# Kernel optimization log

Measured on AMD Instinct MI355X. Metric: run time of the kernel, lower is better.

Reference implementation:

```python
import jax, jax.numpy as jnp
import numpy as np

HIDDEN = 1024
HEADS = 16
HEAD_DIM = HIDDEN // HEADS
NEG_INF = -1.0e9


def setup_inputs() -> dict:
    key = jax.random.key(0)
    ks = jax.random.split(key, 9)
    B, S = 4, 2048
    scale = 1.0 / np.sqrt(HIDDEN)
    inp = {
        'query': jax.random.normal(ks[0], (B, S, HIDDEN), dtype=jnp.float32),
        'masks': jnp.ones((B, S), dtype=jnp.float32),
        'Wq': jax.random.normal(ks[1], (HIDDEN, HIDDEN), dtype=jnp.float32) * scale,
        'bq': jnp.zeros((HIDDEN,), dtype=jnp.float32),
        'Wk': jax.random.normal(ks[2], (HIDDEN, HIDDEN), dtype=jnp.float32) * scale,
        'bk': jnp.zeros((HIDDEN,), dtype=jnp.float32),
        'Wv': jax.random.normal(ks[3], (HIDDEN, HIDDEN), dtype=jnp.float32) * scale,
        'bv': jnp.zeros((HIDDEN,), dtype=jnp.float32),
        'Wo': jax.random.normal(ks[4], (HIDDEN, HIDDEN), dtype=jnp.float32) * scale,
        'bo': jnp.zeros((HIDDEN,), dtype=jnp.float32),
    }
    return inp


def _split_heads(x):
    # [B, S, H*D] -> [B, H, S, D]
    B, S, C = x.shape
    return x.reshape(B, S, HEADS, C // HEADS).transpose(0, 2, 1, 3)


def reference(query, masks, Wq, bq, Wk, bk, Wv, bv, Wo, bo):
    # torch Linear: y = x @ W.T + b
    q = query @ Wq.T + bq
    k = query @ Wk.T + bk
    v = query @ Wv.T + bv
    qh = _split_heads(q) * (HEAD_DIM ** -0.5)  # [B,H,S,D]
    kh = _split_heads(k)
    vh = _split_heads(v)
    bias = ((1.0 - masks) * NEG_INF)[:, None, None, :]  # [B,1,1,S]
    logits = jnp.einsum('bhqd,bhkd->bhqk', qh, kh) + bias
    weights = jax.nn.softmax(logits, axis=-1)  # dropout p=0.0 -> identity
    x = jnp.einsum('bhqk,bhkd->bhqd', weights, vh)  # [B,H,S,D]
    B, H, S, D = x.shape
    combined = x.transpose(0, 2, 1, 3).reshape(B, S, H * D)
    return combined @ Wo.T + bo
```

## Files before the change

### kernel.cpp

```cpp
#include <hip/hip_runtime.h>

typedef unsigned short u16;
typedef unsigned int u32;
typedef u16 u16x4 __attribute__((ext_vector_type(4)));
typedef u16 u16x8 __attribute__((ext_vector_type(8)));
typedef u32 u32x4 __attribute__((ext_vector_type(4)));
typedef __bf16 bf16x8 __attribute__((ext_vector_type(8)));
typedef float f32x4 __attribute__((ext_vector_type(4)));

#define GPTR(p) (const __attribute__((address_space(1))) void*)(p)
#define LPTR(p) (__attribute__((address_space(3))) void*)(p)
#define ASYNC16(g, l) __builtin_amdgcn_global_load_lds(GPTR(g), LPTR(l), 16, 0, 0)

#if __has_builtin(__builtin_amdgcn_exp2f)
#define EXP2(x) __builtin_amdgcn_exp2f(x)
#else
#define EXP2(x) __builtin_exp2f(x)
#endif

__device__ __forceinline__ u16 f2bf(float f) {
    u32 u = __builtin_bit_cast(u32, f);
    return (u16)((u + 0x7fffu + ((u >> 16) & 1u)) >> 16);
}
__device__ __forceinline__ bf16x8 ld8(const void* p) {
    return __builtin_bit_cast(bf16x8, *(const u16x8*)p);
}

__global__ void cvt_all(const float* __restrict__ q,
                        const float* __restrict__ wq, const float* __restrict__ wk,
                        const float* __restrict__ wv, const float* __restrict__ wo,
                        u16* __restrict__ xb, u16* __restrict__ wcat, u16* __restrict__ wob) {
    const int blk = blockIdx.x;
    const float* src;
    u16* dst;
    size_t base;
    if (blk < 8192) {
        src = q; dst = xb; base = (size_t)blk * 256;
    } else {
        const int t = blk - 8192;
        const int w = t >> 10;
        base = (size_t)(t & 1023) * 256;
        src = (w == 0) ? wq : (w == 1) ? wk : (w == 2) ? wv : wo;
        dst = (w == 0) ? wcat : (w == 1) ? wcat + 1024 * 1024
            : (w == 2) ? wcat + 2 * 1024 * 1024 : wob;
    }
    const size_t i = base + threadIdx.x;
    float4 v = ((const float4*)src)[i];
    ushort4 o4;
    o4.x = f2bf(v.x); o4.y = f2bf(v.y); o4.z = f2bf(v.z); o4.w = f2bf(v.w);
    ((ushort4*)dst)[i] = o4;
}

template<int MODE>
__global__ __launch_bounds__(256, 2) void gemm_bt(
    const u16* __restrict__ A, const u16* __restrict__ B,
    const float* __restrict__ b0, const float* __restrict__ b1, const float* __restrict__ b2,
    u16* __restrict__ O0, u16* __restrict__ O1, u16* __restrict__ O2,
    float* __restrict__ OF)
{
    constexpr int K = 1024;
    __shared__ __align__(16) u16 As[128 * 32];
    __shared__ __align__(16) u16 Bs[128 * 32];
    const int tid = threadIdx.x;
    const int wave = tid >> 6, lane = tid & 63;
    const int m0 = blockIdx.y * 128, n0 = blockIdx.x * 128;
    const int wm = (wave >> 1) * 64, wn = (wave & 1) * 64;
    const int fr = lane & 15, fg = lane >> 4;

    f32x4 acc[4][4] = {};

    const int srow = lane >> 2;
    const int scol = (lane & 3) * 8;
    const u16* aSrc = A + (size_t)(m0 + wave * 32 + srow) * K + scol;
    const u16* bSrc = B + (size_t)(n0 + wave * 32 + srow) * K + scol;
    u16* const aDst0 = &As[(wave * 32) * 32];
    u16* const aDst1 = &As[(wave * 32 + 16) * 32];
    u16* const bDst0 = &Bs[(wave * 32) * 32];
    u16* const bDst1 = &Bs[(wave * 32 + 16) * 32];

    for (int kt = 0; kt < K; kt += 32) {
        ASYNC16(aSrc + kt,          aDst0);
        ASYNC16(aSrc + kt + 16 * K, aDst1);
        ASYNC16(bSrc + kt,          bDst0);
        ASYNC16(bSrc + kt + 16 * K, bDst1);
        __syncthreads();
        bf16x8 af[4], bfv[4];
        #pragma unroll
        for (int i = 0; i < 4; ++i) af[i]  = ld8(&As[(wm + i * 16 + fr) * 32 + fg * 8]);
        #pragma unroll
        for (int j = 0; j < 4; ++j) bfv[j] = ld8(&Bs[(wn + j * 16 + fr) * 32 + fg * 8]);
        #pragma unroll
        for (int i = 0; i < 4; ++i)
            #pragma unroll
            for (int j = 0; j < 4; ++j)
                acc[i][j] = __builtin_amdgcn_mfma_f32_16x16x32_bf16(af[i], bfv[j], acc[i][j], 0, 0, 0);
        __syncthreads();
    }

    if constexpr (MODE == 0) {
        const float QSCALE = 0.125f * 1.44269504f;
        #pragma unroll
        for (int j = 0; j < 4; ++j) {
            const int n = n0 + wn + j * 16 + fr;
            const int sel = n >> 10;
            const int w = n & 1023;
            const float bb = (sel == 0 ? b0 : sel == 1 ? b1 : b2)[w];
            const int h = w >> 6, d = w & 63;
            if (sel == 2) {
                #pragma unroll
                for (int i = 0; i < 4; ++i) {
                    const int m = m0 + wm + i * 16 + fg * 4;
                    u16x4 st;
                    #pragma unroll
                    for (int r = 0; r < 4; ++r) st[r] = f2bf(acc[i][j][r] + bb);
                    *(u16x4*)&O2[((size_t)(((m >> 11) * 16 + h) * 64 + d)) * 2048 + (m & 2047)] = st;
                }
            } else {
                const float scale = (sel == 0) ? QSCALE : 1.0f;
                u16* const dst = (sel == 0 ? O0 : O1);
                #pragma unroll
                for (int i = 0; i < 4; ++i) {
                    #pragma unroll
                    for (int r = 0; r < 4; ++r) {
                        const int m = m0 + wm + i * 16 + fg * 4 + r;
                        dst[(((size_t)((m >> 11) * 16 + h) * 2048 + (m & 2047)) << 6) + d] =
                            f2bf((acc[i][j][r] + bb) * scale);
                    }
                }
            }
        }
    } else {
        #pragma unroll
        for (int j = 0; j < 4; ++j) {
            const int n = n0 + wn + j * 16 + fr;
            const float bb = b0[n];
            #pragma unroll
            for (int i = 0; i < 4; ++i) {
                #pragma unroll
                for (int r = 0; r < 4; ++r) {
                    const int m = m0 + wm + i * 16 + fg * 4 + r;
                    OF[(size_t)m * 1024 + n] = acc[i][j][r] + bb;
                }
            }
        }
    }
}

template<bool MASKED>
__device__ __forceinline__ void kv_loop(
    char* smem, const u16* __restrict__ Kbh, const u16* __restrict__ Vtbh,
    const float* __restrict__ mrow, int wave, int fg, int a0, int a1, int t0,
    int srow, int scb, bf16x8 (&qf)[2][2], f32x4 (&o)[4][2], f32x4 (&den)[2],
    const f32x4& FZ, const bf16x8& ONES)
{
    auto STAGE = [&](int buf, int kv0) {
        #pragma unroll
        for (int j = 0; j < 2; ++j) {
            const int r0 = wave * 16 + j * 8;
            const int row = r0 + srow;
            const int sw = scb ^ ((row & 7) << 4);
            ASYNC16((const char*)(Kbh + (size_t)(kv0 + row) * 64) + sw,
                    smem + buf * 8192 + r0 * 128);
            ASYNC16((const char*)(Vtbh + (size_t)row * 2048 + kv0) + sw,
                    smem + 16384 + buf * 8192 + r0 * 128);
        }
    };

    STAGE(0, t0 * 64);
    for (int it = 0; it < 32; it += 2) {
        #pragma unroll
        for (int half = 0; half < 2; ++half) {
            const int tile = (t0 + it + half) & 31;
            const int kv = tile * 64;
            const int kb = half * 8192;
            const int vb = 16384 + half * 8192;
            __syncthreads();
            if (it + half < 31) STAGE(half ^ 1, ((tile + 1) & 31) * 64);

            float4 mv[4];
            if (MASKED) {
                #pragma unroll
                for (int nj = 0; nj < 4; ++nj)
                    mv[nj] = *(const float4*)(mrow + kv + nj * 16 + fg * 4);
            }

            #pragma unroll
            for (int hh = 0; hh < 2; ++hh) {
                const int aK = hh ? a1 : a0;
                f32x4 s[2][2];
                #pragma unroll
                for (int njl = 0; njl < 2; ++njl) {
                    const int nj = hh * 2 + njl;
                    bf16x8 k0 = ld8(smem + kb + nj * 2048 + a0);
                    bf16x8 k1 = ld8(smem + kb + nj * 2048 + a1);
                    __builtin_amdgcn_s_setprio(1);
                    #pragma unroll
                    for (int qs = 0; qs < 2; ++qs) {
                        f32x4 z = __builtin_amdgcn_mfma_f32_16x16x32_bf16(k0, qf[qs][0], FZ, 0, 0, 0);
                        s[njl][qs] = __builtin_amdgcn_mfma_f32_16x16x32_bf16(k1, qf[qs][1], z, 0, 0, 0);
                    }
                    __builtin_amdgcn_s_setprio(0);
                }
                #pragma unroll
                for (int njl = 0; njl < 2; ++njl) {
                    const int nj = hh * 2 + njl;
                    #pragma unroll
                    for (int qs = 0; qs < 2; ++qs)
                        #pragma unroll
                        for (int r = 0; r < 4; ++r) {
                            float p = EXP2(s[njl][qs][r]);
                            if (MASKED) p *= mv[nj][r];
                            s[njl][qs][r] = p;
                        }
                }
                bf16x8 pa[2];
                #pragma unroll
                for (int qs = 0; qs < 2; ++qs) {
                    u32 m0, m1, m2, m3;
                    asm("v_cvt_pk_bf16_f32 %0, %1, %2" : "=v"(m0) : "v"(s[0][qs][0]), "v"(s[0][qs][1]));
                    asm("v_cvt_pk_bf16_f32 %0, %1, %2" : "=v"(m1) : "v"(s[0][qs][2]), "v"(s[0][qs][3]));
                    asm("v_cvt_pk_bf16_f32 %0, %1, %2" : "=v"(m2) : "v"(s[1][qs][0]), "v"(s[1][qs][1]));
                    asm("v_cvt_pk_bf16_f32 %0, %1, %2" : "=v"(m3) : "v"(s[1][qs][2]), "v"(s[1][qs][3]));
                    asm("v_permlane32_swap_b32 %0, %1" : "+v"(m0), "+v"(m2));
                    asm("v_permlane32_swap_b32 %0, %1" : "+v"(m1), "+v"(m3));
                    asm("v_permlane16_swap_b32 %0, %1" : "+v"(m0), "+v"(m2));
                    asm("v_permlane16_swap_b32 %0, %1" : "+v"(m1), "+v"(m3));
                    pa[qs] = __builtin_bit_cast(bf16x8, u32x4{m0, m1, m2, m3});
                }

                __builtin_amdgcn_s_setprio(1);
                #pragma unroll
                for (int qs = 0; qs < 2; ++qs)
                    den[qs] = __builtin_amdgcn_mfma_f32_16x16x32_bf16(ONES, pa[qs], den[qs], 0, 0, 0);
                #pragma unroll
                for (int dj = 0; dj < 4; ++dj) {
                    bf16x8 v = ld8(smem + vb + dj * 2048 + aK);
                    #pragma unroll
                    for (int qs = 0; qs < 2; ++qs)
                        o[dj][qs] = __builtin_amdgcn_mfma_f32_16x16x32_bf16(v, pa[qs], o[dj][qs], 0, 0, 0);
                }
                __builtin_amdgcn_s_setprio(0);
            }
        }
    }
}

__global__ __launch_bounds__(256, 4) void attn_fwd(
    const u16* __restrict__ Qg, const u16* __restrict__ Kg, const u16* __restrict__ Vt,
    const float* __restrict__ masks, u16* __restrict__ X2)
{
    __shared__ __align__(16) char smem[32768];
    const int tid = threadIdx.x;
    const int wave = tid >> 6, lane = tid & 63;

    const int bidL = blockIdx.x;
    const int wg = ((bidL & 7) << 7) | (bidL >> 3);
    const int bh = wg >> 4;
    const int q0 = (wg & 15) * 128 + wave * 32;
    const int b = bh >> 4, h = bh & 15;
    const int fr = lane & 15, fg = lane >> 4;
    const int swz = (fr & 7) << 4;

    const int a0 = fr * 128 + ((fg * 16) ^ swz);
    const int a1 = fr * 128 + ((64 + fg * 16) ^ swz);

    const u16* const Kbh  = Kg + (size_t)bh * 2048 * 64;
    const u16* const Vtbh = Vt + (size_t)bh * 64 * 2048;
    const float* mrow = masks + b * 2048;

    bf16x8 qf[2][2];
    #pragma unroll
    for (int qs = 0; qs < 2; ++qs) {
        const u16* qp = Qg + ((size_t)bh * 2048 + q0 + qs * 16 + fr) * 64 + fg * 8;
        qf[qs][0] = ld8(qp);
        qf[qs][1] = ld8(qp + 32);
    }

    bool ok = true;
    {
        const float4* mp = (const float4*)mrow;
        #pragma unroll
        for (int i = 0; i < 8; ++i) {
            float4 m = mp[lane + i * 64];
            ok = ok && (m.x == 1.0f) && (m.y == 1.0f) && (m.z == 1.0f) && (m.w == 1.0f);
        }
        ok = __all(ok);
    }

    f32x4 o[4][2] = {};
    f32x4 den[2] = {};
    const f32x4 FZ = {0.f, 0.f, 0.f, 0.f};
    const u16x8 ONE_BITS = {0x3F80,0x3F80,0x3F80,0x3F80,0x3F80,0x3F80,0x3F80,0x3F80};
    const bf16x8 ONES = __builtin_bit_cast(bf16x8, ONE_BITS);

    const int srow = lane >> 3;
    const int scb = (lane & 7) * 16;

    const int t0 = (((bidL >> 8) & 3) << 3);

    if (ok)
        kv_loop<false>(smem, Kbh, Vtbh, mrow, wave, fg, a0, a1, t0, srow, scb,
                       qf, o, den, FZ, ONES);
    else
        kv_loop<true>(smem, Kbh, Vtbh, mrow, wave, fg, a0, a1, t0, srow, scb,
                      qf, o, den, FZ, ONES);

    #pragma unroll
    for (int qs = 0; qs < 2; ++qs) {
        const float inv = 1.0f / den[qs][0];
        const int q = q0 + qs * 16 + fr;
        u16* dst = X2 + ((size_t)(b * 2048 + q)) * 1024 + h * 64 + fg * 4;
        #pragma unroll
        for (int dj = 0; dj < 4; ++dj) {
            u16x4 st;
            #pragma unroll
            for (int r = 0; r < 4; ++r) st[r] = f2bf(o[dj][qs][r] * inv);
            *(u16x4*)(dst + dj * 16) = st;
        }
    }
}

extern "C" void kernel_launch(void* const* d_in, const int* in_sizes, int n_in,
                              void* d_out, int out_size, void* d_ws, size_t ws_size,
                              hipStream_t stream) {
    const float* query = (const float*)d_in[0];
    const float* masks = (const float*)d_in[1];
    const float* Wq = (const float*)d_in[2];
    const float* bq = (const float*)d_in[3];
    const float* Wk = (const float*)d_in[4];
    const float* bk = (const float*)d_in[5];
    const float* Wv = (const float*)d_in[6];
    const float* bv = (const float*)d_in[7];
    const float* Wo = (const float*)d_in[8];
    const float* bo = (const float*)d_in[9];
    float* out = (float*)d_out;

    char* ws = (char*)d_ws;
    u16* Xb   = (u16*)(ws);
    u16* Wcat = (u16*)(ws + (16u << 20));
    u16* Wob  = (u16*)(ws + (22u << 20));
    u16* Qg   = (u16*)(ws + (24u << 20));
    u16* Kg   = (u16*)(ws + (40u << 20));
    u16* Vt   = (u16*)(ws + (56u << 20));
    u16* X2   = Xb;

    cvt_all<<<12288, 256, 0, stream>>>(query, Wq, Wk, Wv, Wo, Xb, Wcat, Wob);
    gemm_bt<0><<<dim3(24, 64), 256, 0, stream>>>(Xb, Wcat, bq, bk, bv, Qg, Kg, Vt, nullptr);
    attn_fwd<<<1024, 256, 0, stream>>>(Qg, Kg, Vt, masks, X2);
    gemm_bt<1><<<dim3(8, 64), 256, 0, stream>>>(X2, Wob, bo, nullptr, nullptr, nullptr,
                                                nullptr, nullptr, out);
}
```

Baseline: 186.6 us.

## Load K fragments directly from global into registers, stage only V in LDS

K tiles are no longer staged through shared memory. Each lane loads its K MFMA fragments straight from global memory into registers and prefetches the next tile's fragments after the QK MFMAs. Only V stays in double-buffered LDS, which halves the shared-memory footprint and removes the K LDS reads. The cost is extra VGPRs to hold K fragments, redundant global loads of K across the four waves (served by cache), and global-load latency sitting on the critical path.

Measured after the change: 241.1 us. 29.2% more time.

```diff
diff --git a/kernel.cpp b/kernel.cpp
--- a/kernel.cpp
+++ b/kernel.cpp
@@ -149,33 +149,42 @@
 template<bool MASKED>
 __device__ __forceinline__ void kv_loop(
     char* smem, const u16* __restrict__ Kbh, const u16* __restrict__ Vtbh,
-    const float* __restrict__ mrow, int wave, int fg, int a0, int a1, int t0,
-    int srow, int scb, bf16x8 (&qf)[2][2], f32x4 (&o)[4][2], f32x4 (&den)[2],
-    const f32x4& FZ, const bf16x8& ONES)
+    const float* __restrict__ mrow, int wave, int fr, int fg, int a0, int a1,
+    int t0, int srow, int scb, bf16x8 (&qf)[2][2], f32x4 (&o)[4][2],
+    f32x4 (&den)[2], const f32x4& FZ, const bf16x8& ONES)
 {
-    auto STAGE = [&](int buf, int kv0) {
+    auto STAGE_V = [&](int buf, int kv0) {
         #pragma unroll
         for (int j = 0; j < 2; ++j) {
             const int r0 = wave * 16 + j * 8;
             const int row = r0 + srow;
             const int sw = scb ^ ((row & 7) << 4);
-            ASYNC16((const char*)(Kbh + (size_t)(kv0 + row) * 64) + sw,
+            ASYNC16((const char*)(Vtbh + (size_t)row * 2048 + kv0) + sw,
                     smem + buf * 8192 + r0 * 128);
-            ASYNC16((const char*)(Vtbh + (size_t)row * 2048 + kv0) + sw,
-                    smem + 16384 + buf * 8192 + r0 * 128);
         }
     };
 
-    STAGE(0, t0 * 64);
+    const u16* const kbase = Kbh + (size_t)fr * 64 + fg * 8;
+
+    bf16x8 kk[4][2];
+    #pragma unroll
+    for (int nj = 0; nj < 4; ++nj) {
+        const u16* kp = kbase + (size_t)(t0 * 64 + nj * 16) * 64;
+        kk[nj][0] = ld8(kp);
+        kk[nj][1] = ld8(kp + 32);
+    }
+    STAGE_V(0, t0 * 64);
+
     for (int it = 0; it < 32; it += 2) {
         #pragma unroll
         for (int half = 0; half < 2; ++half) {
             const int tile = (t0 + it + half) & 31;
             const int kv = tile * 64;
-            const int kb = half * 8192;
-            const int vb = 16384 + half * 8192;
+            const int nkv = ((tile + 1) & 31) * 64;
+            const bool pref = (it + half) < 31;
+            const int vb = half * 8192;
             __syncthreads();
-            if (it + half < 31) STAGE(half ^ 1, ((tile + 1) & 31) * 64);
+            if (pref) STAGE_V(half ^ 1, nkv);
 
             float4 mv[4];
             if (MASKED) {
@@ -188,18 +197,25 @@
             for (int hh = 0; hh < 2; ++hh) {
                 const int aK = hh ? a1 : a0;
                 f32x4 s[2][2];
+                __builtin_amdgcn_s_setprio(1);
                 #pragma unroll
                 for (int njl = 0; njl < 2; ++njl) {
                     const int nj = hh * 2 + njl;
-                    bf16x8 k0 = ld8(smem + kb + nj * 2048 + a0);
-                    bf16x8 k1 = ld8(smem + kb + nj * 2048 + a1);
-                    __builtin_amdgcn_s_setprio(1);
                     #pragma unroll
                     for (int qs = 0; qs < 2; ++qs) {
-                        f32x4 z = __builtin_amdgcn_mfma_f32_16x16x32_bf16(k0, qf[qs][0], FZ, 0, 0, 0);
-                        s[njl][qs] = __builtin_amdgcn_mfma_f32_16x16x32_bf16(k1, qf[qs][1], z, 0, 0, 0);
+                        f32x4 z = __builtin_amdgcn_mfma_f32_16x16x32_bf16(kk[nj][0], qf[qs][0], FZ, 0, 0, 0);
+                        s[njl][qs] = __builtin_amdgcn_mfma_f32_16x16x32_bf16(kk[nj][1], qf[qs][1], z, 0, 0, 0);
                     }
-                    __builtin_amdgcn_s_setprio(0);
+                }
+                __builtin_amdgcn_s_setprio(0);
+                if (pref) {
+                    #pragma unroll
+                    for (int njl = 0; njl < 2; ++njl) {
+                        const int nj = hh * 2 + njl;
+                        const u16* kp = kbase + (size_t)(nkv + nj * 16) * 64;
+                        kk[nj][0] = ld8(kp);
+                        kk[nj][1] = ld8(kp + 32);
+                    }
                 }
                 #pragma unroll
                 for (int njl = 0; njl < 2; ++njl) {
@@ -249,7 +265,7 @@
     const u16* __restrict__ Qg, const u16* __restrict__ Kg, const u16* __restrict__ Vt,
     const float* __restrict__ masks, u16* __restrict__ X2)
 {
-    __shared__ __align__(16) char smem[32768];
+    __shared__ __align__(16) char smem[16384];
     const int tid = threadIdx.x;
     const int wave = tid >> 6, lane = tid & 63;
 
@@ -299,10 +315,10 @@
     const int t0 = (((bidL >> 8) & 3) << 3);
 
     if (ok)
-        kv_loop<false>(smem, Kbh, Vtbh, mrow, wave, fg, a0, a1, t0, srow, scb,
+        kv_loop<false>(smem, Kbh, Vtbh, mrow, wave, fr, fg, a0, a1, t0, srow, scb,
                        qf, o, den, FZ, ONES);
     else
-        kv_loop<true>(smem, Kbh, Vtbh, mrow, wave, fg, a0, a1, t0, srow, scb,
+        kv_loop<true>(smem, Kbh, Vtbh, mrow, wave, fr, fg, a0, a1, t0, srow, scb,
                       qf, o, den, FZ, ONES);
 
     #pragma unroll
```
